# Kernel tuning notes

Hardware: AMD Instinct MI355X
Metric: run time of the kernel (lower is better)

Reference implementation:

```python
import jax, jax.numpy as jnp
import numpy as np

N_NODES = 50000
N_EDGES = 800000
D_FEAT = 128
HEADS = 8
UNITS = 32
LEAKY_ALPHA = 0.2  # tf.nn.leaky_relu default
EPS = 1e-7


def setup_inputs() -> dict:
    key = jax.random.key(0)
    k1, k2, k3, k4, k5 = jax.random.split(key, 5)
    x = jax.random.normal(k1, (N_NODES, D_FEAT), dtype=jnp.float32)
    edges = jax.random.randint(k2, (N_EDGES, 2), 0, N_NODES, dtype=jnp.int32)
    kernel = jax.random.normal(k3, (D_FEAT, HEADS * UNITS), dtype=jnp.float32) * (1.0 / np.sqrt(D_FEAT))
    ka1 = jax.random.normal(k4, (1, HEADS, UNITS), dtype=jnp.float32) * (1.0 / np.sqrt(UNITS))
    ka2 = jax.random.normal(k5, (1, HEADS, UNITS), dtype=jnp.float32) * (1.0 / np.sqrt(UNITS))
    bias = jnp.zeros((HEADS * UNITS,), dtype=jnp.float32)
    return {"x": x, "edges": edges, "kernel": kernel, "ka1": ka1, "ka2": ka2, "bias": bias}


def reference(x, edges, kernel, ka1, ka2, bias):
    # x: [N, F]; edges: [E, 2] with columns (source, target)
    n_nodes = x.shape[0]
    targets = edges[:, 1]
    sources = edges[:, 0]

    h = (x @ kernel).reshape(-1, HEADS, UNITS)  # [N, H, U]

    f_t = jnp.sum(h * ka1, axis=-1)[targets]  # [E, H]
    # Faithful to source: f_s gathers from the EDGE-level f_t by source ids
    # (original code overwrites the ka2-based node scores), so ka2 is unused.
    f_s = f_t[sources]  # [E, H]

    scores = jax.nn.leaky_relu(f_t + f_s, negative_slope=LEAKY_ALPHA)  # [E, H]
    seg_max = jax.ops.segment_max(scores, targets, num_segments=n_nodes)
    scores = jnp.exp(scores - seg_max[targets])
    denom = jax.ops.segment_sum(scores, targets, num_segments=n_nodes) + EPS
    scores = scores / denom[targets]  # segment softmax over incoming edges

    out = jax.ops.segment_sum(scores[..., None] * h[sources], targets, num_segments=n_nodes)  # [N, H, U]
    out = out.reshape(n_nodes, HEADS * UNITS)  # concat merge
    return jax.nn.elu(out + bias)
```

## Files before the change

kernel.cpp:

```cpp
#include <hip/hip_runtime.h>
#include <hip/hip_fp16.h>

#define N_NODES 50000
#define N_EDGES 800000
#define D_FEAT 128
#define HEADS 8
#define UNITS 32
#define HU (HEADS * UNITS)
#define LEAKY 0.2f
#define EPSV 1e-7f
#define NBLK 196
#define HSP 258

typedef _Float16 half8 __attribute__((ext_vector_type(8)));
typedef float f32x4 __attribute__((ext_vector_type(4)));

struct h4pk { __half2 a, b; };

#define WBLK 128
__global__ __launch_bounds__(256) void k_wt(const float* __restrict__ W,
                                            __half* __restrict__ Wt,
                                            int* __restrict__ counts) {
    const int i = blockIdx.x * 256 + threadIdx.x;
    const int n = i >> 7, k = i & 127;
    Wt[i] = __float2half(W[k * HU + n]);
    for (int j = i; j < N_NODES; j += WBLK * 256) counts[j] = 0;
}

#define GB 1563
#define CB 12500
__global__ __launch_bounds__(64) void k_big(const float* __restrict__ x,
                                            const __half* __restrict__ Wt,
                                            const float* __restrict__ ka1,
                                            const int* __restrict__ edges,
                                            int* __restrict__ counts,
                                            int* __restrict__ rank,
                                            __half* __restrict__ h,
                                            float* __restrict__ f) {
    __shared__ __align__(16) _Float16 hs[16 * HSP];
    const int l = threadIdx.x;
    if (blockIdx.x >= GB) {
        const int e = (blockIdx.x - GB) * 64 + l;
        if (e < N_EDGES) {
            const int tgt = edges[2 * e + 1];
            rank[e] = atomicAdd(&counts[tgt], 1);
        }
        return;
    }
    const int row16 = l & 15, kg = l >> 4;
    const int rbase = blockIdx.x * 32;

    half8 a0[4], a1[4];
    const int r0 = min(rbase + row16, N_NODES - 1);
    const int r1 = min(rbase + 16 + row16, N_NODES - 1);
    const float* xp0 = x + (size_t)r0 * D_FEAT + kg * 8;
    const float* xp1 = x + (size_t)r1 * D_FEAT + kg * 8;
#pragma unroll
    for (int ks = 0; ks < 4; ++ks) {
        const float4 u0 = *reinterpret_cast<const float4*>(xp0 + ks * 32);
        const float4 v0 = *reinterpret_cast<const float4*>(xp0 + ks * 32 + 4);
        const float4 u1 = *reinterpret_cast<const float4*>(xp1 + ks * 32);
        const float4 v1 = *reinterpret_cast<const float4*>(xp1 + ks * 32 + 4);
        half8 t0, t1;
        t0[0] = (_Float16)u0.x; t0[1] = (_Float16)u0.y; t0[2] = (_Float16)u0.z; t0[3] = (_Float16)u0.w;
        t0[4] = (_Float16)v0.x; t0[5] = (_Float16)v0.y; t0[6] = (_Float16)v0.z; t0[7] = (_Float16)v0.w;
        t1[0] = (_Float16)u1.x; t1[1] = (_Float16)u1.y; t1[2] = (_Float16)u1.z; t1[3] = (_Float16)u1.w;
        t1[4] = (_Float16)v1.x; t1[5] = (_Float16)v1.y; t1[6] = (_Float16)v1.z; t1[7] = (_Float16)v1.w;
        a0[ks] = t0; a1[ks] = t1;
    }

    f32x4 acc0[16], acc1[16];
#pragma unroll
    for (int ct = 0; ct < 16; ++ct) {
        acc0[ct] = (f32x4){0.f, 0.f, 0.f, 0.f};
        acc1[ct] = (f32x4){0.f, 0.f, 0.f, 0.f};
    }

#pragma unroll
    for (int ct = 0; ct < 16; ++ct) {
        const __half* wp = Wt + (ct * 16 + row16) * D_FEAT + kg * 8;
#pragma unroll
        for (int ks = 0; ks < 4; ++ks) {
            const half8 bf = *reinterpret_cast<const half8*>(wp + ks * 32);
            acc0[ct] = __builtin_amdgcn_mfma_f32_16x16x32_f16(a0[ks], bf, acc0[ct], 0, 0, 0);
            acc1[ct] = __builtin_amdgcn_mfma_f32_16x16x32_f16(a1[ks], bf, acc1[ct], 0, 0, 0);
        }
    }

#pragma unroll
    for (int tile = 0; tile < 2; ++tile) {
        const int rb2 = rbase + tile * 16;
#pragma unroll
        for (int ct = 0; ct < 16; ++ct) {
            const int col = ct * 16 + row16;
#pragma unroll
            for (int r = 0; r < 4; ++r) {
                const f32x4 av = tile ? acc1[ct] : acc0[ct];
                hs[(kg * 4 + r) * HSP + col] = (_Float16)av[r];
            }
        }
        __syncthreads();

#pragma unroll
        for (int j = 0; j < 8; ++j) {
            const int slot = j * 64 + l;
            const int row = slot >> 5, c8 = slot & 31;
            if (rb2 + row < N_NODES) {
                const half8 v = *reinterpret_cast<const half8*>(&hs[row * HSP + c8 * 8]);
                *reinterpret_cast<half8*>(h + (size_t)(rb2 + row) * HU + c8 * 8) = v;
            }
        }

#pragma unroll
        for (int hf = 0; hf < 2; ++hf) {
            const int o = hf * 64 + l;
            const int row = o >> 3, hd = o & 7;
            if (rb2 + row < N_NODES) {
                const _Float16* hp = &hs[row * HSP + hd * UNITS];
                const float* kp = ka1 + hd * UNITS;
                float s = 0.f;
#pragma unroll
                for (int u = 0; u < UNITS; u += 8) {
                    const half8 hv = *reinterpret_cast<const half8*>(hp + u);
                    const float4 k0 = *reinterpret_cast<const float4*>(kp + u);
                    const float4 k1 = *reinterpret_cast<const float4*>(kp + u + 4);
                    s += (float)hv[0] * k0.x + (float)hv[1] * k0.y + (float)hv[2] * k0.z + (float)hv[3] * k0.w;
                    s += (float)hv[4] * k1.x + (float)hv[5] * k1.y + (float)hv[6] * k1.z + (float)hv[7] * k1.w;
                }
                f[(size_t)rb2 * HEADS + o] = s;
            }
        }
        __syncthreads();
    }
}

__global__ __launch_bounds__(256) void k_scanA(const int* __restrict__ counts,
                                               int* __restrict__ partials) {
    const int i = blockIdx.x * 256 + threadIdx.x;
    int v = (i < N_NODES) ? counts[i] : 0;
#pragma unroll
    for (int m = 32; m >= 1; m >>= 1) v += __shfl_xor(v, m);
    __shared__ int ws[4];
    if ((threadIdx.x & 63) == 0) ws[threadIdx.x >> 6] = v;
    __syncthreads();
    if (threadIdx.x == 0) partials[blockIdx.x] = ws[0] + ws[1] + ws[2] + ws[3];
}

__global__ __launch_bounds__(256) void k_scanC(const int* __restrict__ counts,
                                               const int* __restrict__ partials,
                                               const int* __restrict__ edges,
                                               const float* __restrict__ f,
                                               int* __restrict__ offs,
                                               float* __restrict__ g) {
    __shared__ int sp[256];
    __shared__ int s[256];
    const int t = threadIdx.x;

    sp[t] = (t < NBLK) ? partials[t] : 0;
    __syncthreads();
    for (int o = 1; o < 256; o <<= 1) {
        const int u = (t >= o) ? sp[t - o] : 0;
        __syncthreads();
        sp[t] += u;
        __syncthreads();
    }
    const int prefix = (blockIdx.x > 0) ? sp[blockIdx.x - 1] : 0;

    const int i = blockIdx.x * 256 + t;
    const int v = (i < N_NODES) ? counts[i] : 0;
    s[t] = v;
    __syncthreads();
    for (int o = 1; o < 256; o <<= 1) {
        const int u = (t >= o) ? s[t - o] : 0;
        __syncthreads();
        s[t] += u;
        __syncthreads();
    }
    if (i < N_NODES) {
        offs[i] = prefix + s[t] - v;
        const int t2 = edges[2 * i + 1];
        const float4 A = *reinterpret_cast<const float4*>(f + (size_t)t2 * HEADS);
        const float4 B = *reinterpret_cast<const float4*>(f + (size_t)t2 * HEADS + 4);
        *reinterpret_cast<float4*>(g + (size_t)i * HEADS) = A;
        *reinterpret_cast<float4*>(g + (size_t)i * HEADS + 4) = B;
    }
}

#define EBLK 3125
__global__ __launch_bounds__(256) void k_fill(const int* __restrict__ edges,
                                              const int* __restrict__ offs,
                                              const int* __restrict__ rank,
                                              int* __restrict__ elist) {
    const int e = blockIdx.x * 256 + threadIdx.x;
    if (e >= N_EDGES) return;
    const int2 st = reinterpret_cast<const int2*>(edges)[e];
    elist[offs[st.y] + rank[e]] = st.x;
}

__global__ __launch_bounds__(256) void k_out(const __half* __restrict__ h,
                                             const int* __restrict__ elist,
                                             const float* __restrict__ f,
                                             const float* __restrict__ g,
                                             const int* __restrict__ offs,
                                             const int* __restrict__ counts,
                                             const float* __restrict__ bias,
                                             float* __restrict__ out,
                                             int nbase, int ncount) {
    const int ni = blockIdx.x * 4 + (threadIdx.x >> 6);
    if (ni >= ncount) return;
    const int n = nbase + ni;
    const int lane = threadIdx.x & 63;
    const int head = lane >> 3;
    const int c4 = lane * 4;
    const int start = offs[n];
    const int end = start + counts[n];
    const float fn = f[(size_t)n * HEADS + head];

    float d = 0.f;
    float4 acc = make_float4(0.f, 0.f, 0.f, 0.f);

    int p = start;
    for (; p + 8 <= end; p += 8) {
        int ss[8];
#pragma unroll
        for (int j = 0; j < 8; ++j) ss[j] = elist[p + j];
        float gz[8];
#pragma unroll
        for (int j = 0; j < 8; ++j) gz[j] = g[(size_t)ss[j] * HEADS + head];
        h4pk hv[8];
#pragma unroll
        for (int j = 0; j < 8; ++j) hv[j] = *reinterpret_cast<const h4pk*>(h + (size_t)ss[j] * HU + c4);
#pragma unroll
        for (int j = 0; j < 8; ++j) {
            float z = fn + gz[j];
            z = (z > 0.f) ? z : LEAKY * z;
            const float w = __expf(z);
            d += w;
            const float2 fa = __half22float2(hv[j].a);
            const float2 fb = __half22float2(hv[j].b);
            acc.x += w * fa.x; acc.y += w * fa.y; acc.z += w * fb.x; acc.w += w * fb.y;
        }
    }
    for (; p + 4 <= end; p += 4) {
        int ss[4];
#pragma unroll
        for (int j = 0; j < 4; ++j) ss[j] = elist[p + j];
        float gz[4];
#pragma unroll
        for (int j = 0; j < 4; ++j) gz[j] = g[(size_t)ss[j] * HEADS + head];
        h4pk hv[4];
#pragma unroll
        for (int j = 0; j < 4; ++j) hv[j] = *reinterpret_cast<const h4pk*>(h + (size_t)ss[j] * HU + c4);
#pragma unroll
        for (int j = 0; j < 4; ++j) {
            float z = fn + gz[j];
            z = (z > 0.f) ? z : LEAKY * z;
            const float w = __expf(z);
            d += w;
            const float2 fa = __half22float2(hv[j].a);
            const float2 fb = __half22float2(hv[j].b);
            acc.x += w * fa.x; acc.y += w * fa.y; acc.z += w * fb.x; acc.w += w * fb.y;
        }
    }
    for (; p < end; ++p) {
        const int s = elist[p];
        float z = fn + g[(size_t)s * HEADS + head];
        z = (z > 0.f) ? z : LEAKY * z;
        const float w = __expf(z);
        const h4pk hv = *reinterpret_cast<const h4pk*>(h + (size_t)s * HU + c4);
        const float2 fa = __half22float2(hv.a);
        const float2 fb = __half22float2(hv.b);
        d += w;
        acc.x += w * fa.x;
        acc.y += w * fa.y;
        acc.z += w * fb.x;
        acc.w += w * fb.y;
    }

    const float inv = 1.f / (d + EPSV);
    const float4 b = *reinterpret_cast<const float4*>(bias + c4);
    float v;
    float4 o;
    v = acc.x * inv + b.x; o.x = (v > 0.f) ? v : expm1f(v);
    v = acc.y * inv + b.y; o.y = (v > 0.f) ? v : expm1f(v);
    v = acc.z * inv + b.z; o.z = (v > 0.f) ? v : expm1f(v);
    v = acc.w * inv + b.w; o.w = (v > 0.f) ? v : expm1f(v);
    *reinterpret_cast<float4*>(out + (size_t)n * HU + c4) = o;
}

extern "C" void kernel_launch(void* const* d_in, const int* in_sizes, int n_in,
                              void* d_out, int out_size, void* d_ws, size_t ws_size,
                              hipStream_t stream) {
    const float* x = (const float*)d_in[0];
    const int* edges = (const int*)d_in[1];
    const float* W = (const float*)d_in[2];
    const float* ka1 = (const float*)d_in[3];
    const float* bias = (const float*)d_in[5];
    float* out = (float*)d_out;

    char* ws = (char*)d_ws;
    size_t off = 0;
    auto alloc = [&](size_t bytes) -> void* {
        void* p = ws + off;
        off = (off + bytes + 255) & ~size_t(255);
        return p;
    };
    __half* h = (__half*)alloc(sizeof(__half) * (size_t)N_NODES * HU);
    __half* Wt = (__half*)alloc(sizeof(__half) * D_FEAT * HU);
    float* f = (float*)alloc(sizeof(float) * N_NODES * HEADS);
    float* g = (float*)alloc(sizeof(float) * N_NODES * HEADS);
    int* counts = (int*)alloc(sizeof(int) * N_NODES);
    int* offs = (int*)alloc(sizeof(int) * N_NODES);
    int* partials = (int*)alloc(sizeof(int) * NBLK);
    int* rank = (int*)alloc(sizeof(int) * N_EDGES);
    int* elist = (int*)alloc(sizeof(int) * N_EDGES);

    k_wt<<<WBLK, 256, 0, stream>>>(W, Wt, counts);
    k_big<<<GB + CB, 64, 0, stream>>>(x, Wt, ka1, edges, counts, rank, h, f);
    k_scanA<<<NBLK, 256, 0, stream>>>(counts, partials);
    k_scanC<<<NBLK, 256, 0, stream>>>(counts, partials, edges, f, offs, g);
    k_fill<<<EBLK, 256, 0, stream>>>(edges, offs, rank, elist);
    k_out<<<(25000 + 3) / 4, 256, 0, stream>>>(h, elist, f, g, offs, counts, bias, out, 0, 25000);
    k_out<<<(25000 + 3) / 4, 256, 0, stream>>>(h, elist, f, g, offs, counts, bias, out, 25000, 25000);
}
```

Before: 151.1 us.

## Drop LDS staging in GEMM epilogue; compute head scores with shuffles

```diff
diff --git a/kernel.cpp b/kernel.cpp
--- a/kernel.cpp
+++ b/kernel.cpp
@@ -10,7 +10,6 @@
 #define LEAKY 0.2f
 #define EPSV 1e-7f
 #define NBLK 196
-#define HSP 258
 
 typedef _Float16 half8 __attribute__((ext_vector_type(8)));
 typedef float f32x4 __attribute__((ext_vector_type(4)));
@@ -28,7 +27,7 @@
 }
 
 #define GB 1563
-#define CB 12500
+#define CB 3125
 __global__ __launch_bounds__(64) void k_big(const float* __restrict__ x,
                                             const __half* __restrict__ Wt,
                                             const float* __restrict__ ka1,
@@ -37,13 +36,16 @@
                                             int* __restrict__ rank,
                                             __half* __restrict__ h,
                                             float* __restrict__ f) {
-    __shared__ __align__(16) _Float16 hs[16 * HSP];
     const int l = threadIdx.x;
     if (blockIdx.x >= GB) {
-        const int e = (blockIdx.x - GB) * 64 + l;
-        if (e < N_EDGES) {
-            const int tgt = edges[2 * e + 1];
-            rank[e] = atomicAdd(&counts[tgt], 1);
+        const int base = (blockIdx.x - GB) * 256;
+#pragma unroll
+        for (int j = 0; j < 4; ++j) {
+            const int e = base + j * 64 + l;
+            if (e < N_EDGES) {
+                const int tgt = edges[2 * e + 1];
+                rank[e] = atomicAdd(&counts[tgt], 1);
+            }
         }
         return;
     }
@@ -93,44 +95,33 @@
 #pragma unroll
         for (int ct = 0; ct < 16; ++ct) {
             const int col = ct * 16 + row16;
+            const f32x4 av = tile ? acc1[ct] : acc0[ct];
 #pragma unroll
             for (int r = 0; r < 4; ++r) {
-                const f32x4 av = tile ? acc1[ct] : acc0[ct];
-                hs[(kg * 4 + r) * HSP + col] = (_Float16)av[r];
+                const int hr = rb2 + kg * 4 + r;
+                if (hr < N_NODES)
+                    h[(size_t)hr * HU + col] = __float2half(av[r]);
             }
         }
-        __syncthreads();
-
-#pragma unroll
-        for (int j = 0; j < 8; ++j) {
-            const int slot = j * 64 + l;
-            const int row = slot >> 5, c8 = slot & 31;
-            if (rb2 + row < N_NODES) {
-                const half8 v = *reinterpret_cast<const half8*>(&hs[row * HSP + c8 * 8]);
-                *reinterpret_cast<half8*>(h + (size_t)(rb2 + row) * HU + c8 * 8) = v;
+#pragma unroll
+        for (int hd = 0; hd < 8; ++hd) {
+            const float ka = ka1[hd * 32 + row16];
+            const float kb = ka1[hd * 32 + 16 + row16];
+            const f32x4 ae = tile ? acc1[2 * hd] : acc0[2 * hd];
+            const f32x4 ao = tile ? acc1[2 * hd + 1] : acc0[2 * hd + 1];
+#pragma unroll
+            for (int r = 0; r < 4; ++r) {
+                float v = ae[r] * ka + ao[r] * kb;
+                v += __shfl_xor(v, 1);
+                v += __shfl_xor(v, 2);
+                v += __shfl_xor(v, 4);
+                v += __shfl_xor(v, 8);
+                if (row16 == 0) {
+                    const int hr = rb2 + kg * 4 + r;
+                    if (hr < N_NODES) f[(size_t)hr * HEADS + hd] = v;
+                }
             }
         }
-
-#pragma unroll
-        for (int hf = 0; hf < 2; ++hf) {
-            const int o = hf * 64 + l;
-            const int row = o >> 3, hd = o & 7;
-            if (rb2 + row < N_NODES) {
-                const _Float16* hp = &hs[row * HSP + hd * UNITS];
-                const float* kp = ka1 + hd * UNITS;
-                float s = 0.f;
-#pragma unroll
-                for (int u = 0; u < UNITS; u += 8) {
-                    const half8 hv = *reinterpret_cast<const half8*>(hp + u);
-                    const float4 k0 = *reinterpret_cast<const float4*>(kp + u);
-                    const float4 k1 = *reinterpret_cast<const float4*>(kp + u + 4);
-                    s += (float)hv[0] * k0.x + (float)hv[1] * k0.y + (float)hv[2] * k0.z + (float)hv[3] * k0.w;
-                    s += (float)hv[4] * k1.x + (float)hv[5] * k1.y + (float)hv[6] * k1.z + (float)hv[7] * k1.w;
-                }
-                f[(size_t)rb2 * HEADS + o] = s;
-            }
-        }
-        __syncthreads();
     }
 }
 
```

Measured after the change: 148.0 us. 2.0% less time.

## Partition aggregation gathers into source-range passes and batch edge counting per block

Applied to the files above, without the earlier changes.

```diff
diff --git a/kernel.cpp b/kernel.cpp
--- a/kernel.cpp
+++ b/kernel.cpp
@@ -10,7 +10,8 @@
 #define LEAKY 0.2f
 #define EPSV 1e-7f
 #define NBLK 196
-#define HSP 258
+#define HSP 260
+#define NPASS 8
 
 typedef _Float16 half8 __attribute__((ext_vector_type(8)));
 typedef float f32x4 __attribute__((ext_vector_type(4)));
@@ -28,7 +29,7 @@
 }
 
 #define GB 1563
-#define CB 12500
+#define CB 3125
 __global__ __launch_bounds__(64) void k_big(const float* __restrict__ x,
                                             const __half* __restrict__ Wt,
                                             const float* __restrict__ ka1,
@@ -40,10 +41,14 @@
     __shared__ __align__(16) _Float16 hs[16 * HSP];
     const int l = threadIdx.x;
     if (blockIdx.x >= GB) {
-        const int e = (blockIdx.x - GB) * 64 + l;
-        if (e < N_EDGES) {
-            const int tgt = edges[2 * e + 1];
-            rank[e] = atomicAdd(&counts[tgt], 1);
+        const int base = (blockIdx.x - GB) * 256;
+#pragma unroll
+        for (int j = 0; j < 4; ++j) {
+            const int e = base + j * 64 + l;
+            if (e < N_EDGES) {
+                const int tgt = edges[2 * e + 1];
+                rank[e] = atomicAdd(&counts[tgt], 1);
+            }
         }
         return;
     }
@@ -197,15 +202,74 @@
     elist[offs[st.y] + rank[e]] = st.x;
 }
 
-__global__ __launch_bounds__(256) void k_out(const __half* __restrict__ h,
-                                             const int* __restrict__ elist,
-                                             const float* __restrict__ f,
-                                             const float* __restrict__ g,
-                                             const int* __restrict__ offs,
-                                             const int* __restrict__ counts,
-                                             const float* __restrict__ bias,
-                                             float* __restrict__ out,
-                                             int nbase, int ncount) {
+__global__ __launch_bounds__(256) void k_outA(const __half* __restrict__ h,
+                                              const int* __restrict__ elist,
+                                              const float* __restrict__ f,
+                                              const float* __restrict__ g,
+                                              const int* __restrict__ offs,
+                                              const int* __restrict__ counts,
+                                              const float* __restrict__ bias,
+                                              float* __restrict__ out,
+                                              int nbase, int ncount) {
+    const int ni = blockIdx.x * 4 + (threadIdx.x >> 6);
+    if (ni >= ncount) return;
+    const int n = nbase + ni;
+    const int lane = threadIdx.x & 63;
+    const int head = lane >> 3;
+    const int c4 = lane * 4;
+    const int start = offs[n];
+    const int end = start + counts[n];
+    const float fn = f[(size_t)n * HEADS + head];
+
+    float d = 0.f;
+    float4 acc = make_float4(0.f, 0.f, 0.f, 0.f);
+
+    for (int pass = 0; pass < NPASS; ++pass) {
+        const int lo = pass * (N_NODES / NPASS);
+        const int hi = lo + (N_NODES / NPASS);
+        for (int p = start; p < end; p += 8) {
+            int ss[8];
+#pragma unroll
+            for (int j = 0; j < 8; ++j)
+                ss[j] = elist[(p + j < end) ? (p + j) : (end - 1)];
+#pragma unroll
+            for (int j = 0; j < 8; ++j) {
+                if (p + j >= end) break;
+                const int s = ss[j];
+                if (s < lo || s >= hi) continue;
+                const float gz = g[(size_t)s * HEADS + head];
+                const h4pk hv = *reinterpret_cast<const h4pk*>(h + (size_t)s * HU + c4);
+                float z = fn + gz;
+                z = (z > 0.f) ? z : LEAKY * z;
+                const float w = __expf(z);
+                d += w;
+                const float2 fa = __half22float2(hv.a);
+                const float2 fb = __half22float2(hv.b);
+                acc.x += w * fa.x; acc.y += w * fa.y; acc.z += w * fb.x; acc.w += w * fb.y;
+            }
+        }
+    }
+
+    const float inv = 1.f / (d + EPSV);
+    const float4 b = *reinterpret_cast<const float4*>(bias + c4);
+    float v;
+    float4 o;
+    v = acc.x * inv + b.x; o.x = (v > 0.f) ? v : expm1f(v);
+    v = acc.y * inv + b.y; o.y = (v > 0.f) ? v : expm1f(v);
+    v = acc.z * inv + b.z; o.z = (v > 0.f) ? v : expm1f(v);
+    v = acc.w * inv + b.w; o.w = (v > 0.f) ? v : expm1f(v);
+    *reinterpret_cast<float4*>(out + (size_t)n * HU + c4) = o;
+}
+
+__global__ __launch_bounds__(256) void k_outB(const __half* __restrict__ h,
+                                              const int* __restrict__ elist,
+                                              const float* __restrict__ f,
+                                              const float* __restrict__ g,
+                                              const int* __restrict__ offs,
+                                              const int* __restrict__ counts,
+                                              const float* __restrict__ bias,
+                                              float* __restrict__ out,
+                                              int nbase, int ncount) {
     const int ni = blockIdx.x * 4 + (threadIdx.x >> 6);
     if (ni >= ncount) return;
     const int n = nbase + ni;
@@ -320,6 +384,6 @@
     k_scanA<<<NBLK, 256, 0, stream>>>(counts, partials);
     k_scanC<<<NBLK, 256, 0, stream>>>(counts, partials, edges, f, offs, g);
     k_fill<<<EBLK, 256, 0, stream>>>(edges, offs, rank, elist);
-    k_out<<<(25000 + 3) / 4, 256, 0, stream>>>(h, elist, f, g, offs, counts, bias, out, 0, 25000);
-    k_out<<<(25000 + 3) / 4, 256, 0, stream>>>(h, elist, f, g, offs, counts, bias, out, 25000, 25000);
-}
+    k_outA<<<(25000 + 3) / 4, 256, 0, stream>>>(h, elist, f, g, offs, counts, bias, out, 0, 25000);
+    k_outB<<<(25000 + 3) / 4, 256, 0, stream>>>(h, elist, f, g, offs, counts, bias, out, 25000, 25000);
+}
```

New measurement: 210.7 us. +39.4%, slower.
